# Kernel optimization log

Measured on AMD Instinct MI355X. Metric: run time of the kernel, lower is better.

Reference implementation:

```python
import jax, jax.numpy as jnp
import numpy as np
from jax import lax

B, T, H, M, K, Q, P = 32, 128, 256, 1000, 3, 4, 2  # batch, phones, hidden, max_mel_len, kernel, q_out, p_out


def _ln(x, g, b, eps=1e-5):
    mu = jnp.mean(x, -1, keepdims=True)
    var = jnp.mean((x - mu) ** 2, -1, keepdims=True)
    return (x - mu) * lax.rsqrt(var + eps) * g + b


def _forward(x, x_mask, x_dur, params):
    (proj_w, proj_b, conv_w, conv_b, conv_g, conv_beta,
     q_w1, q_b1, q_g, q_beta, q_w2, q_b2,
     p_w1, p_b1, p_g, p_beta, p_w2, p_b2,
     proj1_w, proj1_b, proj2_w, proj2_b, projo_w, projo_b) = params

    valid = (~x_mask).astype(x.dtype)[:, :, None]                      # (B,T,1), 1 = real phone
    # proj -> ConvBlock (shared between the w and c branches; dropout is identity in eval)
    h = x @ proj_w + proj_b                                            # (B,T,H)
    hc = lax.conv_general_dilated((h * valid).transpose(0, 2, 1), conv_w,
                                  (1,), 'SAME',
                                  dimension_numbers=('NCH', 'OIH', 'NCH'))
    hc = hc.transpose(0, 2, 1) + conv_b                                # (B,T,8)
    hc = jax.nn.silu(_ln(hc, conv_g, conv_beta)) * valid               # (B,T,8)

    mel_lens = jnp.minimum(jnp.round(jnp.sum(x_dur, -1)).astype(jnp.int32), M)
    mel_pad = jnp.arange(M)[None, :] >= mel_lens[:, None]              # (B,M) True = padded frame
    mask = x_mask[:, None, :] | mel_pad[:, :, None]                    # (B,M,T)

    e = jnp.cumsum(x_dur, -1)                                          # phone end times
    s = e - x_dur                                                      # phone start times
    t = jnp.arange(1, M + 1, dtype=x.dtype)
    E = jnp.where(mask, 0.0, e[:, None, :] - t[None, :, None])         # (B,M,T)
    S = jnp.where(mask, 0.0, t[None, :, None] - s[:, None, :])         # (B,M,T)

    feat = jnp.concatenate([jnp.broadcast_to(hc[:, None], (B, M, T, 8)),
                            S[..., None], E[..., None]], axis=-1)      # (B,M,T,10)

    # mlp_q scores -> masked softmax over phone axis
    sc = jax.nn.silu(_ln(feat @ q_w1 + q_b1, q_g, q_beta)) @ q_w2 + q_b2   # (B,M,T,Q)
    sc = jnp.where(x_mask[:, None, :, None], -jnp.inf, sc)
    w = jax.nn.softmax(sc, axis=2)
    w = jnp.where(mel_pad[:, :, None, None], 0.0, w)                   # (B,M,T,Q)

    # mlp_p per-(frame,phone) auxiliary features
    c = jax.nn.silu(_ln(feat @ p_w1 + p_b1, p_g, p_beta)) @ p_w2 + p_b2    # (B,M,T,P)

    # dual einsum combine (matches torch permute+view ordering: q-major then feature)
    wh = jnp.einsum('bmnq,bnh->bmqh', w, x).reshape(B, M, Q * H) @ proj1_w + proj1_b
    wc = jnp.einsum('bmnq,bmnp->bmqp', w, c).reshape(B, M, Q * P) @ proj2_w + proj2_b
    o = jnp.where(mel_pad[:, :, None], 0.0, wh + wc) @ projo_w + projo_b   # (B,M,2H)

    mel_mask = jnp.broadcast_to(mel_pad[:, :, None], (B, M, T))
    return o, mel_mask, mel_lens, jnp.transpose(w, (0, 3, 1, 2))


def setup_inputs() -> dict:
    key = jax.random.key(0)
    ks = jax.random.split(key, 16)
    x = jax.random.normal(ks[0], (B, T, H), jnp.float32)
    x_lengths = jax.random.randint(ks[1], (B,), T // 2, T + 1).at[0].set(T)
    x_mask = jnp.arange(T)[None, :] >= x_lengths[:, None]              # True = pad
    x_dur = jax.random.uniform(ks[2], (B, T), jnp.float32, 2.0, 10.0)
    x_dur = x_dur * (~x_mask)
    x_dur = x_dur.at[0].multiply(2.0)  # element 0 total duration > M -> static max_mel_len = M

    def xavier(k, shape):
        return jax.random.normal(k, shape, jnp.float32) * jnp.sqrt(2.0 / (shape[0] + shape[1]))

    return dict(
        x=x, x_mask=x_mask, x_dur=x_dur, x_lengths=x_lengths,
        proj_w=xavier(ks[3], (H, H)), proj_b=jnp.zeros((H,)),
        conv_w=jax.random.normal(ks[4], (8, H, K), jnp.float32) * 0.05, conv_b=jnp.zeros((8,)),
        conv_g=jnp.ones((8,)), conv_beta=jnp.zeros((8,)),
        q_w1=xavier(ks[5], (10, Q)), q_b1=jnp.zeros((Q,)),
        q_g=jnp.ones((Q,)), q_beta=jnp.zeros((Q,)),
        q_w2=xavier(ks[6], (Q, Q)), q_b2=jnp.zeros((Q,)),
        p_w1=xavier(ks[7], (10, P)), p_b1=jnp.zeros((P,)),
        p_g=jnp.ones((P,)), p_beta=jnp.zeros((P,)),
        p_w2=xavier(ks[8], (P, P)), p_b2=jnp.zeros((P,)),
        proj1_w=xavier(ks[9], (H * Q, H)), proj1_b=jnp.zeros((H,)),
        proj2_w=xavier(ks[10], (Q * P, H)), proj2_b=jnp.zeros((H,)),
        projo_w=xavier(ks[11], (H, 2 * H)), projo_b=jnp.zeros((2 * H,)),
    )


def reference(x, x_mask, x_dur, x_lengths,
              proj_w, proj_b, conv_w, conv_b, conv_g, conv_beta,
              q_w1, q_b1, q_g, q_beta, q_w2, q_b2,
              p_w1, p_b1, p_g, p_beta, p_w2, p_b2,
              proj1_w, proj1_b, proj2_w, proj2_b, projo_w, projo_b):
    params = (proj_w, proj_b, conv_w, conv_b, conv_g, conv_beta,
              q_w1, q_b1, q_g, q_beta, q_w2, q_b2,
              p_w1, p_b1, p_g, p_beta, p_w2, p_b2,
              proj1_w, proj1_b, proj2_w, proj2_b, projo_w, projo_b)
    return _forward(x, x_mask, x_dur, params)
```

## Files before the change

### kernel.cpp

```cpp
#include <hip/hip_runtime.h>
#include <math.h>

#define BB 32
#define TT 128
#define HH 256
#define MM 1000

typedef __attribute__((ext_vector_type(8))) short short8;
typedef __attribute__((ext_vector_type(4))) float floatx4;

__device__ inline void fma4(float4& a, const float4 b, float s) {
    a.x += b.x * s; a.y += b.y * s; a.z += b.z * s; a.w += b.w * s;
}

__device__ inline unsigned short f2bf(float f) {
    union { float f; unsigned int u; } c; c.f = f;
    unsigned int u = c.u;
    return (unsigned short)((u + 0x7FFFu + ((u >> 16) & 1u)) >> 16);
}

__device__ inline float bf2f(unsigned short h) {
    union { unsigned int u; float f; } c; c.u = ((unsigned int)h) << 16; return c.f;
}


__global__ void k_prep(const float* __restrict__ dur, float* __restrict__ e_cum,
                       int* __restrict__ ml_i, float* __restrict__ ml_out,
                       unsigned short* __restrict__ w_bf) {
    int b = blockIdx.x;
    int tid = threadIdx.x;
    #pragma unroll
    for (int q = 0; q < 4; ++q) {
        uint4* dst = (uint4*)(w_bf + (((size_t)(b * 4 + q)) * 1024 + 1000) * 128);
        for (int e = tid; e < 384; e += 64) dst[e] = make_uint4(0, 0, 0, 0);
    }
    if (tid == 0) {
        float run = 0.f;
        const float* d = dur + b * TT;
        float* e = e_cum + b * TT;
        for (int t = 0; t < TT; ++t) { run += d[t]; e[t] = run; }
        int ml = (int)rintf(run);
        if (ml > MM) ml = MM;
        if (ml < 0) ml = 0;
        ml_i[b] = ml;
        ml_out[b] = (float)ml;
    }
}

__global__ __launch_bounds__(256) void k_h(const float* __restrict__ x,
                                           const float* __restrict__ pw,
                                           const float* __restrict__ pb,
                                           float* __restrict__ h) {
    __shared__ float xs[16][HH];
    int blk = blockIdx.x;
    int b = blk >> 3, tt = blk & 7;
    int t0 = tt * 16;
    int tid = threadIdx.x;
    for (int e = tid; e < 16 * HH; e += 256) {
        int r = e >> 8, i = e & 255;
        xs[r][i] = x[(b * TT + t0 + r) * HH + i];
    }
    __syncthreads();
    int jg = tid & 63, rg = tid >> 6;
    int j4 = jg * 4;
    float4 bias = *(const float4*)(pb + j4);
    float4 acc[4];
    #pragma unroll
    for (int ri = 0; ri < 4; ++ri) acc[ri] = bias;
    #pragma unroll 4
    for (int i = 0; i < HH; ++i) {
        float4 wv = *(const float4*)(pw + i * HH + j4);
        #pragma unroll
        for (int ri = 0; ri < 4; ++ri) fma4(acc[ri], wv, xs[rg * 4 + ri][i]);
    }
    #pragma unroll
    for (int ri = 0; ri < 4; ++ri)
        *(float4*)(h + (b * TT + t0 + rg * 4 + ri) * HH + j4) = acc[ri];
}

__global__ __launch_bounds__(128) void k_conv(const float* __restrict__ h,
                                              const float* __restrict__ cw,
                                              const int* __restrict__ xlen,
                                              float* __restrict__ hcpre) {
    __shared__ float hs[18][257];
    __shared__ float cws[8][769];
    int blk = blockIdx.x;
    int b = blk >> 3, tt = blk & 7;
    int t0 = tt * 16;
    int tid = threadIdx.x;
    int L = xlen[b];
    for (int e = tid; e < 18 * 256; e += 128) {
        int r = e >> 8, i = e & 255;
        int t = t0 - 1 + r;
        float v = 0.f;
        if (t >= 0 && t < TT && t < L) v = h[((size_t)b * TT + t) * HH + i];
        hs[r][i] = v;
    }
    for (int e = tid; e < 6144; e += 128) {
        int o = e / 768, rem = e - o * 768;
        cws[o][rem] = cw[e];
    }
    __syncthreads();
    int o = tid >> 4, tl = tid & 15;
    float acc = 0.f;
    #pragma unroll
    for (int k = 0; k < 3; ++k) {
        const float* wr = &cws[o][k];
        const float* hr = hs[tl + k];
        #pragma unroll 8
        for (int i = 0; i < 256; ++i) acc += hr[i] * wr[i * 3];
    }
    hcpre[((size_t)b * TT + t0 + tl) * 8 + o] = acc;
}

__global__ __launch_bounds__(128) void k_bases(
    const float* __restrict__ hcpre, const float* __restrict__ cb,
    const float* __restrict__ cg, const float* __restrict__ cbeta,
    const float* __restrict__ qw1, const float* __restrict__ qb1,
    const float* __restrict__ pw1, const float* __restrict__ pb1,
    const float* __restrict__ e_cum, const float* __restrict__ dur,
    const int* __restrict__ xlen,
    float* __restrict__ baseq, float* __restrict__ basep) {
    int b = blockIdx.x;
    int t = threadIdx.x;
    int L = xlen[b];
    float v[8];
    float mu = 0.f;
    #pragma unroll
    for (int o = 0; o < 8; ++o) { v[o] = hcpre[(b * TT + t) * 8 + o] + cb[o]; mu += v[o]; }
    mu *= 0.125f;
    float var = 0.f;
    #pragma unroll
    for (int o = 0; o < 8; ++o) { float d = v[o] - mu; var += d * d; }
    var *= 0.125f;
    float rs = 1.0f / sqrtf(var + 1e-5f);
    float valid = (t < L) ? 1.f : 0.f;
    #pragma unroll
    for (int o = 0; o < 8; ++o) {
        float a = (v[o] - mu) * rs * cg[o] + cbeta[o];
        v[o] = a / (1.f + expf(-a)) * valid;
    }
    float e = e_cum[b * TT + t];
    float s_ = e - dur[b * TT + t];
    #pragma unroll
    for (int j = 0; j < 4; ++j) {
        float acc = qb1[j];
        #pragma unroll
        for (int o = 0; o < 8; ++o) acc += v[o] * qw1[o * 4 + j];
        acc += e * qw1[9 * 4 + j] - s_ * qw1[8 * 4 + j];
        baseq[(b * TT + t) * 4 + j] = acc;
    }
    #pragma unroll
    for (int j = 0; j < 2; ++j) {
        float acc = pb1[j];
        #pragma unroll
        for (int o = 0; o < 8; ++o) acc += v[o] * pw1[o * 2 + j];
        acc += e * pw1[9 * 2 + j] - s_ * pw1[8 * 2 + j];
        basep[(b * TT + t) * 2 + j] = acc;
    }
}

__global__ __launch_bounds__(256) void k_wsoft(
    const float* __restrict__ baseq, const float* __restrict__ basep,
    const float* __restrict__ qw1, const float* __restrict__ qg,
    const float* __restrict__ qbeta, const float* __restrict__ qw2,
    const float* __restrict__ qb2,
    const float* __restrict__ pw1, const float* __restrict__ pg,
    const float* __restrict__ pbeta, const float* __restrict__ pw2,
    const float* __restrict__ pb2,
    const int* __restrict__ xlen, const int* __restrict__ ml_i,
    float* __restrict__ w_out, float* __restrict__ mm_out,
    float* __restrict__ wc8, unsigned short* __restrict__ w_bf) {
    int blk = blockIdx.x;
    int b = blk / 250;
    int mg = blk - b * 250;
    int wv = threadIdx.x >> 6, lane = threadIdx.x & 63;
    int m = mg * 4 + wv;
    int ml = ml_i[b];
    int t1 = lane, t2 = lane + 64;
    bool pad = (m >= ml);
    size_t mmbase = ((size_t)b * MM + m) * TT;
    mm_out[mmbase + t1] = pad ? 1.f : 0.f;
    mm_out[mmbase + t2] = pad ? 1.f : 0.f;
    if (pad) {
        #pragma unroll
        for (int q = 0; q < 4; ++q) {
            size_t wb = ((size_t)(b * 4 + q) * MM + m) * TT;
            w_out[wb + t1] = 0.f;
            w_out[wb + t2] = 0.f;
            unsigned short* wbq = w_bf + (((size_t)(b * 4 + q)) * 1024 + m) * 128;
            wbq[t1] = 0; wbq[t2] = 0;
        }
        if (lane == 0) {
            #pragma unroll
            for (int r = 0; r < 8; ++r) wc8[((size_t)b * MM + m) * 8 + r] = 0.f;
        }
        return;
    }
    int L = xlen[b];
    float mp1 = (float)(m + 1);
    float dq[4];
    #pragma unroll
    for (int j = 0; j < 4; ++j) dq[j] = mp1 * (qw1[8 * 4 + j] - qw1[9 * 4 + j]);

    float sc1[4], sc2[4];
    float c1v[2], c2v[2];
    #pragma unroll
    for (int half = 0; half < 2; ++half) {
        int t = half ? t2 : t1;
        float* sc = half ? sc2 : sc1;
        float* cv = half ? c2v : c1v;
        if (t < L) {
            float4 bq = *(const float4*)(baseq + ((size_t)b * TT + t) * 4);
            float z[4] = {bq.x + dq[0], bq.y + dq[1], bq.z + dq[2], bq.w + dq[3]};
            float mu = 0.25f * (z[0] + z[1] + z[2] + z[3]);
            float var = 0.f;
            #pragma unroll
            for (int j = 0; j < 4; ++j) { float d = z[j] - mu; var += d * d; }
            var *= 0.25f;
            float rs = 1.f / sqrtf(var + 1e-5f);
            float a[4];
            #pragma unroll
            for (int j = 0; j < 4; ++j) {
                float av = (z[j] - mu) * rs * qg[j] + qbeta[j];
                a[j] = av / (1.f + expf(-av));
            }
            #pragma unroll
            for (int q = 0; q < 4; ++q) {
                float s = qb2[q];
                #pragma unroll
                for (int j = 0; j < 4; ++j) s += a[j] * qw2[j * 4 + q];
                sc[q] = s;
            }
            float z0 = basep[((size_t)b * TT + t) * 2 + 0] + mp1 * (pw1[16] - pw1[18]);
            float z1 = basep[((size_t)b * TT + t) * 2 + 1] + mp1 * (pw1[17] - pw1[19]);
            float pmu = 0.5f * (z0 + z1);
            float d0 = z0 - pmu, d1 = z1 - pmu;
            float pvar = 0.5f * (d0 * d0 + d1 * d1);
            float prs = 1.f / sqrtf(pvar + 1e-5f);
            float a0 = d0 * prs * pg[0] + pbeta[0];
            float a1 = d1 * prs * pg[1] + pbeta[1];
            a0 = a0 / (1.f + expf(-a0));
            a1 = a1 / (1.f + expf(-a1));
            cv[0] = pb2[0] + a0 * pw2[0] + a1 * pw2[2];
            cv[1] = pb2[1] + a0 * pw2[1] + a1 * pw2[3];
        } else {
            sc[0] = sc[1] = sc[2] = sc[3] = -__builtin_inff();
            cv[0] = cv[1] = 0.f;
        }
    }
    float w1[4], w2[4];
    #pragma unroll
    for (int q = 0; q < 4; ++q) {
        float mx = fmaxf(sc1[q], sc2[q]);
        #pragma unroll
        for (int off = 32; off > 0; off >>= 1) mx = fmaxf(mx, __shfl_xor(mx, off, 64));
        float e1 = expf(sc1[q] - mx);
        float e2 = expf(sc2[q] - mx);
        float s = e1 + e2;
        #pragma unroll
        for (int off = 32; off > 0; off >>= 1) s += __shfl_xor(s, off, 64);
        w1[q] = e1 / s;
        w2[q] = e2 / s;
        size_t wb = ((size_t)(b * 4 + q) * MM + m) * TT;
        w_out[wb + t1] = w1[q];
        w_out[wb + t2] = w2[q];
        unsigned short* wbq = w_bf + (((size_t)(b * 4 + q)) * 1024 + m) * 128;
        wbq[t1] = f2bf(w1[q]);
        wbq[t2] = f2bf(w2[q]);
    }
    float red[8];
    #pragma unroll
    for (int r8 = 0; r8 < 8; ++r8) {
        int q = r8 >> 1, p = r8 & 1;
        float v = w1[q] * c1v[p] + w2[q] * c2v[p];
        #pragma unroll
        for (int off = 32; off > 0; off >>= 1) v += __shfl_xor(v, off, 64);
        red[r8] = v;
    }
    if (lane == 0) {
        #pragma unroll
        for (int r8 = 0; r8 < 8; ++r8) wc8[((size_t)b * MM + m) * 8 + r8] = red[r8];
    }
}

__global__ __launch_bounds__(256) void k_pw_part(const float* __restrict__ p1w,
                                                 const float* __restrict__ po,
                                                 float* __restrict__ PWpart) {
    __shared__ float S[16][64];
    int blk = blockIdx.x;
    int ks = blk & 3, colT = (blk >> 2) & 7, ht = blk >> 5;
    int q = colT >> 1, j0 = (colT & 1) * 256;
    int h0 = ht * 16, k0 = ks * 64;
    int tid = threadIdx.x;
    for (int e = tid; e < 1024; e += 256) {
        int r = e >> 6, c = e & 63;
        S[r][c] = p1w[(q * 256 + h0 + r) * 256 + k0 + c];
    }
    __syncthreads();
    int jg = tid & 63, rg = tid >> 6;
    int jcol = j0 + jg * 4;
    float4 acc[4];
    #pragma unroll
    for (int r = 0; r < 4; ++r) acc[r] = make_float4(0, 0, 0, 0);
    float4 nb = *(const float4*)(po + (size_t)k0 * 512 + jcol);
    for (int c = 0; c < 64; ++c) {
        float4 cur = nb;
        if (c < 63) nb = *(const float4*)(po + (size_t)(k0 + c + 1) * 512 + jcol);
        #pragma unroll
        for (int r = 0; r < 4; ++r) fma4(acc[r], cur, S[rg * 4 + r][c]);
    }
    #pragma unroll
    for (int r = 0; r < 4; ++r) {
        int hh = h0 + rg * 4 + r;
        *(float4*)(PWpart + (size_t)ks * 524288 + hh * 2048 + q * 512 + jcol) = acc[r];
    }
}

__global__ __launch_bounds__(256) void k_pwt(const float* __restrict__ PWpart,
                                             unsigned short* __restrict__ pwh,
                                             unsigned short* __restrict__ pwl) {
    __shared__ float S[64][65];
    int blk = blockIdx.x;
    int nt = blk & 31, ct = blk >> 5;
    int c0 = ct * 64, n0 = nt * 64;
    int tid = threadIdx.x;
    for (int e = tid; e < 4096; e += 256) {
        int cc = e >> 6, nn = e & 63;
        size_t off = (size_t)(c0 + cc) * 2048 + n0 + nn;
        float v = PWpart[off] + PWpart[524288 + off]
                + PWpart[2 * 524288 + off] + PWpart[3 * 524288 + off];
        S[cc][nn] = v;
    }
    __syncthreads();
    for (int e = tid; e < 4096; e += 256) {
        int nn = e >> 6, cc = e & 63;
        float v = S[cc][nn];
        unsigned short h = f2bf(v);
        size_t d = (size_t)(n0 + nn) * 256 + c0 + cc;
        pwh[d] = h;
        pwl[d] = f2bf(v - bf2f(h));
    }
}

__global__ __launch_bounds__(256) void k_xcvt(const float* __restrict__ x,
                                              unsigned short* __restrict__ xh,
                                              unsigned short* __restrict__ xl) {
    int idx = (blockIdx.x * 256 + threadIdx.x) * 4;
    float4 v = *(const float4*)(x + idx);
    float vv[4] = {v.x, v.y, v.z, v.w};
    union { unsigned short us[4]; uint2 u; } hi, lo;
    #pragma unroll
    for (int k = 0; k < 4; ++k) {
        unsigned short h = f2bf(vv[k]);
        hi.us[k] = h;
        lo.us[k] = f2bf(vv[k] - bf2f(h));
    }
    *(uint2*)(xh + idx) = hi.u;
    *(uint2*)(xl + idx) = lo.u;
}

__global__ __launch_bounds__(512) void k_small(const float* __restrict__ p2w,
    const float* __restrict__ po, const float* __restrict__ p1b,
    const float* __restrict__ p2b, const float* __restrict__ pob,
    float* __restrict__ P2o, float* __restrict__ bvec) {
    int j = threadIdx.x;
    float acc[9];
    #pragma unroll
    for (int r = 0; r < 9; ++r) acc[r] = 0.f;
    for (int c = 0; c < HH; ++c) {
        float pv = po[c * 512 + j];
        #pragma unroll
        for (int r = 0; r < 8; ++r) acc[r] += p2w[r * HH + c] * pv;
        acc[8] += (p1b[c] + p2b[c]) * pv;
    }
    #pragma unroll
    for (int r = 0; r < 8; ++r) P2o[r * 512 + j] = acc[r];
    bvec[j] = acc[8] + pob[j];
}

__device__ inline int swzk(int row, int chunk) {
    return row * 32 + ((chunk ^ ((row >> 1) & 3)) << 3);
}

__global__ __launch_bounds__(256) void k_A2m(const unsigned short* __restrict__ xh,
                                             const unsigned short* __restrict__ xl,
                                             const unsigned short* __restrict__ pwh,
                                             const unsigned short* __restrict__ pwl,
                                             unsigned short* __restrict__ A2T) {
    __shared__ __align__(16) unsigned short SM[16384];
    unsigned short* Ah = SM;
    unsigned short* Al = SM + 4096;
    unsigned short* Bh = SM + 8192;
    unsigned short* Bl = SM + 12288;
    int blk = blockIdx.x;
    int b = blk >> 4, nt = blk & 15;
    int n0 = nt * 128;
    int tid = threadIdx.x;
    int lane = tid & 63, wv = tid >> 6;
    int wm = wv & 1, wn = wv >> 1;

    floatx4 acc[16];
    #pragma unroll
    for (int i = 0; i < 16; ++i) acc[i] = (floatx4){0.f, 0.f, 0.f, 0.f};

    int srow = tid >> 1, shalf = tid & 1;
    const unsigned short* gxh = xh + ((size_t)(b * TT + srow) * 256 + shalf * 16);
    const unsigned short* gxl = xl + ((size_t)(b * TT + srow) * 256 + shalf * 16);
    const unsigned short* gph = pwh + ((size_t)(n0 + srow) * 256 + shalf * 16);
    const unsigned short* gpl = pwl + ((size_t)(n0 + srow) * 256 + shalf * 16);
    int wAd0 = swzk(srow, 2 * shalf);
    int wAd1 = swzk(srow, 2 * shalf + 1);

    int ra = wm * 64 + (lane & 15);
    int rb = wn * 64 + (lane & 15);
    int cq = lane >> 4;

    for (int kc = 0; kc < 256; kc += 32) {
        uint4 a0 = *(const uint4*)(gxh + kc);
        uint4 a1 = *(const uint4*)(gxh + kc + 8);
        uint4 a2 = *(const uint4*)(gxl + kc);
        uint4 a3 = *(const uint4*)(gxl + kc + 8);
        uint4 b0 = *(const uint4*)(gph + kc);
        uint4 b1 = *(const uint4*)(gph + kc + 8);
        uint4 b2 = *(const uint4*)(gpl + kc);
        uint4 b3 = *(const uint4*)(gpl + kc + 8);
        *(uint4*)&Ah[wAd0] = a0; *(uint4*)&Ah[wAd1] = a1;
        *(uint4*)&Al[wAd0] = a2; *(uint4*)&Al[wAd1] = a3;
        *(uint4*)&Bh[wAd0] = b0; *(uint4*)&Bh[wAd1] = b1;
        *(uint4*)&Bl[wAd0] = b2; *(uint4*)&Bl[wAd1] = b3;
        __syncthreads();
        short8 afh[4], afl[4], bfh[4], bfl[4];
        #pragma unroll
        for (int i = 0; i < 4; ++i) {
            afh[i] = *(const short8*)&Ah[swzk(ra + i * 16, cq)];
            afl[i] = *(const short8*)&Al[swzk(ra + i * 16, cq)];
            bfh[i] = *(const short8*)&Bh[swzk(rb + i * 16, cq)];
            bfl[i] = *(const short8*)&Bl[swzk(rb + i * 16, cq)];
        }
        #pragma unroll
        for (int i = 0; i < 4; ++i)
            #pragma unroll
            for (int j = 0; j < 4; ++j) {
                floatx4 c = acc[i * 4 + j];
                c = __builtin_amdgcn_mfma_f32_16x16x32_bf16(afh[i], bfh[j], c, 0, 0, 0);
                c = __builtin_amdgcn_mfma_f32_16x16x32_bf16(afh[i], bfl[j], c, 0, 0, 0);
                c = __builtin_amdgcn_mfma_f32_16x16x32_bf16(afl[i], bfh[j], c, 0, 0, 0);
                acc[i * 4 + j] = c;
            }
        __syncthreads();
    }

    unsigned short* OT = SM;
    #pragma unroll
    for (int i = 0; i < 4; ++i)
        #pragma unroll
        for (int j = 0; j < 4; ++j) {
            int nloc = wn * 64 + j * 16 + (lane & 15);
            int tb = wm * 64 + i * 16 + ((lane >> 4) << 2);
            union { unsigned short us[4]; uint2 v; } pk;
            #pragma unroll
            for (int r = 0; r < 4; ++r) pk.us[r] = f2bf(acc[i * 4 + j][r]);
            int chunk = tb >> 3, sub = tb & 7;
            *(uint2*)&OT[nloc * 128 + (((chunk ^ (nloc & 15)) << 3) | sub)] = pk.v;
        }
    __syncthreads();
    int q = n0 >> 9, jb = n0 & 511;
    for (int u = tid; u < 2048; u += 256) {
        int nrow = u >> 4, seg = u & 15;
        uint4 v = *(const uint4*)&OT[nrow * 128 + ((seg ^ (nrow & 15)) << 3)];
        *(uint4*)(A2T + (((size_t)(b * 4 + q) * 512) + jb + nrow) * 128 + seg * 8) = v;
    }
}

__global__ __launch_bounds__(256, 2) void k_main(
    const unsigned short* __restrict__ w_bf, const unsigned short* __restrict__ A2T,
    const float* __restrict__ wc8, const float* __restrict__ P2o,
    const float* __restrict__ bvec, const float* __restrict__ pob,
    const int* __restrict__ ml_i, float* __restrict__ o_out) {
    __shared__ __align__(16) unsigned short Asm[2][128 * 40];
    __shared__ __align__(16) unsigned short Bsm[2][128 * 40];
    int wgid = blockIdx.x;
    int blk = (wgid & 7) * 128 + (wgid >> 3);
    int nt = blk & 3, mt = (blk >> 2) & 7, b = blk >> 5;
    int m0 = mt * 128, n0 = nt * 128;
    int tid = threadIdx.x;
    int ml = ml_i[b];

    if (m0 >= ml) {
        float* pb_s = (float*)&Asm[0][0];
        if (tid < 128) pb_s[tid] = pob[n0 + tid];
        __syncthreads();
        int col4 = (tid & 31) * 4;
        float4 pv = *(const float4*)&pb_s[col4];
        for (int r = tid >> 5; r < 128; r += 8) {
            int m = m0 + r;
            if (m < MM)
                *(float4*)(o_out + ((size_t)b * MM + m) * 512 + n0 + col4) = pv;
        }
        return;
    }

    int lane = tid & 63, wv = tid >> 6;
    int wm = wv & 1, wn = wv >> 1;

    floatx4 acc[16];
    #pragma unroll
    for (int i = 0; i < 16; ++i) acc[i] = (floatx4){0.f, 0.f, 0.f, 0.f};

    int rl = lane >> 4;
    int cl = lane & 15;
    int ra = wm * 64 + cl;
    int rb = wn * 64 + cl;

    int srow = tid >> 2, schunk = tid & 3;
    int doff = srow * 40 + schunk * 8;
    const size_t bq4 = (size_t)b * 4;

    #pragma unroll
    for (int j = 0; j < 2; ++j) {
        int row = srow + j * 64;
        uint4 va = *(const uint4*)(w_bf + ((bq4 + 0) * 1024 + m0 + row) * 128 + schunk * 8);
        uint4 vb = *(const uint4*)(A2T + ((bq4 + 0) * 512 + n0 + row) * 128 + schunk * 8);
        *(uint4*)&Asm[0][doff + j * 2560] = va;
        *(uint4*)&Bsm[0][doff + j * 2560] = vb;
    }
    __syncthreads();

    int cur = 0;
    for (int s = 0; s < 16; ++s) {
        uint4 la[2], lb[2];
        if (s < 15) {
            int q = (s + 1) >> 2, koff = ((s + 1) & 3) * 32;
            #pragma unroll
            for (int j = 0; j < 2; ++j) {
                int row = srow + j * 64;
                la[j] = *(const uint4*)(w_bf +
                    ((bq4 + q) * 1024 + m0 + row) * 128 + koff + schunk * 8);
                lb[j] = *(const uint4*)(A2T +
                    ((bq4 + q) * 512 + n0 + row) * 128 + koff + schunk * 8);
            }
        }
        {
            int co = rl * 8;
            short8 af[4], bfr[4];
            #pragma unroll
            for (int i = 0; i < 4; ++i)
                af[i] = *(const short8*)&Asm[cur][(ra + i * 16) * 40 + co];
            #pragma unroll
            for (int j2 = 0; j2 < 4; ++j2)
                bfr[j2] = *(const short8*)&Bsm[cur][(rb + j2 * 16) * 40 + co];
            #pragma unroll
            for (int i = 0; i < 4; ++i)
                #pragma unroll
                for (int j2 = 0; j2 < 4; ++j2)
                    acc[i * 4 + j2] = __builtin_amdgcn_mfma_f32_16x16x32_bf16(
                        af[i], bfr[j2], acc[i * 4 + j2], 0, 0, 0);
        }
        if (s < 15) {
            #pragma unroll
            for (int j = 0; j < 2; ++j) {
                *(uint4*)&Asm[cur ^ 1][doff + j * 2560] = la[j];
                *(uint4*)&Bsm[cur ^ 1][doff + j * 2560] = lb[j];
            }
        }
        __syncthreads();
        cur ^= 1;
    }

    float* wc8s = (float*)&Asm[0][0];
    float* P2os = (float*)&Bsm[0][0];
    float* bvs  = (float*)&Bsm[0][0] + 1024;
    float* pobs = (float*)&Bsm[0][0] + 1152;
    for (int e = tid; e < 1024; e += 256) {
        int mm_ = e >> 3, r = e & 7;
        int m = m0 + mm_;
        wc8s[e] = (m < MM) ? wc8[((size_t)b * MM + m) * 8 + r] : 0.f;
    }
    for (int e = tid; e < 1024; e += 256) {
        int r = e >> 7, j = e & 127;
        P2os[e] = P2o[r * 512 + n0 + j];
    }
    if (tid < 128) {
        bvs[tid] = bvec[n0 + tid];
        pobs[tid] = pob[n0 + tid];
    }
    __syncthreads();
    #pragma unroll
    for (int i = 0; i < 4; ++i) {
        #pragma unroll
        for (int j = 0; j < 4; ++j) {
            int nloc = wn * 64 + j * 16 + (lane & 15);
            #pragma unroll
            for (int reg = 0; reg < 4; ++reg) {
                int mloc = wm * 64 + i * 16 + (lane >> 4) * 4 + reg;
                int m = m0 + mloc;
                if (m >= MM) continue;
                float v;
                if (m < ml) {
                    v = acc[i * 4 + j][reg] + bvs[nloc];
                    #pragma unroll
                    for (int r8 = 0; r8 < 8; ++r8)
                        v += wc8s[mloc * 8 + r8] * P2os[r8 * 128 + nloc];
                } else {
                    v = pobs[nloc];
                }
                o_out[((size_t)b * MM + m) * 512 + n0 + nloc] = v;
            }
        }
    }
}

extern "C" void kernel_launch(void* const* d_in, const int* in_sizes, int n_in,
                              void* d_out, int out_size, void* d_ws, size_t ws_size,
                              hipStream_t stream) {
    (void)in_sizes; (void)n_in; (void)out_size; (void)ws_size;
    const float* x      = (const float*)d_in[0];
    const float* dur    = (const float*)d_in[2];
    const int*   xlen   = (const int*)d_in[3];
    const float* proj_w = (const float*)d_in[4];
    const float* proj_b = (const float*)d_in[5];
    const float* conv_w = (const float*)d_in[6];
    const float* conv_b = (const float*)d_in[7];
    const float* conv_g = (const float*)d_in[8];
    const float* conv_be= (const float*)d_in[9];
    const float* q_w1   = (const float*)d_in[10];
    const float* q_b1   = (const float*)d_in[11];
    const float* q_g    = (const float*)d_in[12];
    const float* q_be   = (const float*)d_in[13];
    const float* q_w2   = (const float*)d_in[14];
    const float* q_b2   = (const float*)d_in[15];
    const float* p_w1   = (const float*)d_in[16];
    const float* p_b1   = (const float*)d_in[17];
    const float* p_g    = (const float*)d_in[18];
    const float* p_be   = (const float*)d_in[19];
    const float* p_w2   = (const float*)d_in[20];
    const float* p_b2   = (const float*)d_in[21];
    const float* p1w    = (const float*)d_in[22];
    const float* p1b    = (const float*)d_in[23];
    const float* p2w    = (const float*)d_in[24];
    const float* p2b    = (const float*)d_in[25];
    const float* pow_   = (const float*)d_in[26];
    const float* pob    = (const float*)d_in[27];

    float* ws    = (float*)d_ws;
    float* e_cum = ws + 0;
    float* hcpre = ws + 4096;
    float* baseq = ws + 36864;
    float* basep = ws + 53248;
    float* h     = ws + 61440;
    unsigned short* x_hi = (unsigned short*)(ws + 61440);
    unsigned short* x_lo = (unsigned short*)(ws + 585728);
    unsigned short* pw_h = (unsigned short*)(ws + 1110016);
    unsigned short* pw_l = (unsigned short*)(ws + 1372160);
    unsigned short* A2T = (unsigned short*)(ws + 1634304);
    float* wc8   = ws + 5828608;
    float* P2o   = ws + 6084608;
    float* bvec  = ws + 6088704;
    int*   ml_i  = (int*)(ws + 6089216);
    float* PWpart= ws + 6090752;
    unsigned short* w_bf = (unsigned short*)(ws + 8187904);

    float* o_out  = (float*)d_out;
    float* mm_out = o_out + 16384000;
    float* ml_out = o_out + 20480000;
    float* w_out  = o_out + 20480032;

    k_prep<<<dim3(BB), dim3(64), 0, stream>>>(dur, e_cum, ml_i, ml_out, w_bf);
    k_h<<<dim3(BB * 8), dim3(256), 0, stream>>>(x, proj_w, proj_b, h);
    k_conv<<<dim3(BB * 8), dim3(128), 0, stream>>>(h, conv_w, xlen, hcpre);
    k_xcvt<<<dim3(1024), dim3(256), 0, stream>>>(x, x_hi, x_lo);
    k_bases<<<dim3(BB), dim3(128), 0, stream>>>(hcpre, conv_b, conv_g, conv_be,
                                                q_w1, q_b1, p_w1, p_b1,
                                                e_cum, dur, xlen, baseq, basep);
    k_pw_part<<<dim3(512), dim3(256), 0, stream>>>(p1w, pow_, PWpart);
    k_pwt<<<dim3(128), dim3(256), 0, stream>>>(PWpart, pw_h, pw_l);
    k_small<<<dim3(1), dim3(512), 0, stream>>>(p2w, pow_, p1b, p2b, pob, P2o, bvec);
    k_A2m<<<dim3(512), dim3(256), 0, stream>>>(x_hi, x_lo, pw_h, pw_l, A2T);
    k_wsoft<<<dim3(BB * 250), dim3(256), 0, stream>>>(baseq, basep,
                                                      q_w1, q_g, q_be, q_w2, q_b2,
                                                      p_w1, p_g, p_be, p_w2, p_b2,
                                                      xlen, ml_i, w_out, mm_out, wc8, w_bf);
    k_main<<<dim3(BB * 32), dim3(256), 0, stream>>>(w_bf, A2T, wc8, P2o, bvec,
                                                    pob, ml_i, o_out);
}
```

Before: 397.7 us.

## Merge nine small preprocessing kernels into three block-dispatched launches by dependency level

Independent preprocessing kernels are grouped by dependency level into three kernels (kF1, kF2, kF3) that branch on block index to run the original per-kernel work. This cuts launch count and idle gaps between tiny kernels, and lets independent work such as the proj matmul, the PW partial products, the x conversion and the prep share the GPU at once. The x_hi/x_lo buffers move to a new workspace offset because they previously aliased h, which is now written in the same launch. Shared memory per block becomes the union of the merged kernels, and some branches leave threads idle (e.g., the conv part uses 128 of 256 threads).

```diff
diff --git a/kernel.cpp b/kernel.cpp
--- a/kernel.cpp
+++ b/kernel.cpp
@@ -24,96 +24,197 @@
 }
 
 
-__global__ void k_prep(const float* __restrict__ dur, float* __restrict__ e_cum,
-                       int* __restrict__ ml_i, float* __restrict__ ml_out,
-                       unsigned short* __restrict__ w_bf) {
-    int b = blockIdx.x;
+__global__ __launch_bounds__(256) void kF1(
+    const float* __restrict__ x, const float* __restrict__ pw_h_,
+    const float* __restrict__ pb_h, float* __restrict__ h,
+    const float* __restrict__ p1w, const float* __restrict__ po,
+    float* __restrict__ PWpart,
+    unsigned short* __restrict__ xh, unsigned short* __restrict__ xl,
+    const float* __restrict__ dur, float* __restrict__ e_cum,
+    int* __restrict__ ml_i, float* __restrict__ ml_out,
+    unsigned short* __restrict__ w_bf) {
+    __shared__ __align__(16) float S1[4096];
+    int gb = blockIdx.x;
     int tid = threadIdx.x;
-    #pragma unroll
-    for (int q = 0; q < 4; ++q) {
-        uint4* dst = (uint4*)(w_bf + (((size_t)(b * 4 + q)) * 1024 + 1000) * 128);
-        for (int e = tid; e < 384; e += 64) dst[e] = make_uint4(0, 0, 0, 0);
-    }
-    if (tid == 0) {
-        float run = 0.f;
-        const float* d = dur + b * TT;
-        float* e = e_cum + b * TT;
-        for (int t = 0; t < TT; ++t) { run += d[t]; e[t] = run; }
-        int ml = (int)rintf(run);
-        if (ml > MM) ml = MM;
-        if (ml < 0) ml = 0;
-        ml_i[b] = ml;
-        ml_out[b] = (float)ml;
-    }
-}
-
-__global__ __launch_bounds__(256) void k_h(const float* __restrict__ x,
-                                           const float* __restrict__ pw,
-                                           const float* __restrict__ pb,
-                                           float* __restrict__ h) {
-    __shared__ float xs[16][HH];
-    int blk = blockIdx.x;
-    int b = blk >> 3, tt = blk & 7;
-    int t0 = tt * 16;
+
+    if (gb < 256) {
+        float (*xs)[HH] = (float(*)[HH])S1;
+        int b = gb >> 3, tt = gb & 7;
+        int t0 = tt * 16;
+        for (int e = tid; e < 16 * HH; e += 256) {
+            int r = e >> 8, i = e & 255;
+            xs[r][i] = x[(b * TT + t0 + r) * HH + i];
+        }
+        __syncthreads();
+        int jg = tid & 63, rg = tid >> 6;
+        int j4 = jg * 4;
+        float4 bias = *(const float4*)(pb_h + j4);
+        float4 acc[4];
+        #pragma unroll
+        for (int ri = 0; ri < 4; ++ri) acc[ri] = bias;
+        #pragma unroll 4
+        for (int i = 0; i < HH; ++i) {
+            float4 wv = *(const float4*)(pw_h_ + i * HH + j4);
+            #pragma unroll
+            for (int ri = 0; ri < 4; ++ri) fma4(acc[ri], wv, xs[rg * 4 + ri][i]);
+        }
+        #pragma unroll
+        for (int ri = 0; ri < 4; ++ri)
+            *(float4*)(h + (b * TT + t0 + rg * 4 + ri) * HH + j4) = acc[ri];
+    } else if (gb < 768) {
+        float (*S)[64] = (float(*)[64])S1;
+        int blk = gb - 256;
+        int ks = blk & 3, colT = (blk >> 2) & 7, ht = blk >> 5;
+        int q = colT >> 1, j0 = (colT & 1) * 256;
+        int h0 = ht * 16, k0 = ks * 64;
+        for (int e = tid; e < 1024; e += 256) {
+            int r = e >> 6, c = e & 63;
+            S[r][c] = p1w[(q * 256 + h0 + r) * 256 + k0 + c];
+        }
+        __syncthreads();
+        int jg = tid & 63, rg = tid >> 6;
+        int jcol = j0 + jg * 4;
+        float4 acc[4];
+        #pragma unroll
+        for (int r = 0; r < 4; ++r) acc[r] = make_float4(0, 0, 0, 0);
+        float4 nb = *(const float4*)(po + (size_t)k0 * 512 + jcol);
+        for (int c = 0; c < 64; ++c) {
+            float4 cur = nb;
+            if (c < 63) nb = *(const float4*)(po + (size_t)(k0 + c + 1) * 512 + jcol);
+            #pragma unroll
+            for (int r = 0; r < 4; ++r) fma4(acc[r], cur, S[rg * 4 + r][c]);
+        }
+        #pragma unroll
+        for (int r = 0; r < 4; ++r) {
+            int hh = h0 + rg * 4 + r;
+            *(float4*)(PWpart + (size_t)ks * 524288 + hh * 2048 + q * 512 + jcol) = acc[r];
+        }
+    } else if (gb < 1792) {
+        int idx = ((gb - 768) * 256 + tid) * 4;
+        float4 v = *(const float4*)(x + idx);
+        float vv[4] = {v.x, v.y, v.z, v.w};
+        union { unsigned short us[4]; uint2 u; } hi, lo;
+        #pragma unroll
+        for (int k = 0; k < 4; ++k) {
+            unsigned short hv = f2bf(vv[k]);
+            hi.us[k] = hv;
+            lo.us[k] = f2bf(vv[k] - bf2f(hv));
+        }
+        *(uint2*)(xh + idx) = hi.u;
+        *(uint2*)(xl + idx) = lo.u;
+    } else {
+        int b = gb - 1792;
+        if (tid < 64) {
+            #pragma unroll
+            for (int q = 0; q < 4; ++q) {
+                uint4* dst = (uint4*)(w_bf + (((size_t)(b * 4 + q)) * 1024 + 1000) * 128);
+                for (int e = tid; e < 384; e += 64) dst[e] = make_uint4(0, 0, 0, 0);
+            }
+            if (tid == 0) {
+                float run = 0.f;
+                const float* d = dur + b * TT;
+                float* e = e_cum + b * TT;
+                for (int t = 0; t < TT; ++t) { run += d[t]; e[t] = run; }
+                int ml = (int)rintf(run);
+                if (ml > MM) ml = MM;
+                if (ml < 0) ml = 0;
+                ml_i[b] = ml;
+                ml_out[b] = (float)ml;
+            }
+        }
+    }
+}
+
+__global__ __launch_bounds__(256) void kF2(
+    const float* __restrict__ h, const float* __restrict__ cw,
+    const int* __restrict__ xlen, float* __restrict__ hcpre,
+    const float* __restrict__ PWpart,
+    unsigned short* __restrict__ pwh, unsigned short* __restrict__ pwl,
+    const float* __restrict__ p2w, const float* __restrict__ po,
+    const float* __restrict__ p1b, const float* __restrict__ p2b,
+    const float* __restrict__ pob,
+    float* __restrict__ P2o, float* __restrict__ bvec) {
+    __shared__ __align__(16) float S2[10778];
+    int gb = blockIdx.x;
     int tid = threadIdx.x;
-    for (int e = tid; e < 16 * HH; e += 256) {
-        int r = e >> 8, i = e & 255;
-        xs[r][i] = x[(b * TT + t0 + r) * HH + i];
-    }
-    __syncthreads();
-    int jg = tid & 63, rg = tid >> 6;
-    int j4 = jg * 4;
-    float4 bias = *(const float4*)(pb + j4);
-    float4 acc[4];
-    #pragma unroll
-    for (int ri = 0; ri < 4; ++ri) acc[ri] = bias;
-    #pragma unroll 4
-    for (int i = 0; i < HH; ++i) {
-        float4 wv = *(const float4*)(pw + i * HH + j4);
-        #pragma unroll
-        for (int ri = 0; ri < 4; ++ri) fma4(acc[ri], wv, xs[rg * 4 + ri][i]);
-    }
-    #pragma unroll
-    for (int ri = 0; ri < 4; ++ri)
-        *(float4*)(h + (b * TT + t0 + rg * 4 + ri) * HH + j4) = acc[ri];
-}
-
-__global__ __launch_bounds__(128) void k_conv(const float* __restrict__ h,
-                                              const float* __restrict__ cw,
-                                              const int* __restrict__ xlen,
-                                              float* __restrict__ hcpre) {
-    __shared__ float hs[18][257];
-    __shared__ float cws[8][769];
-    int blk = blockIdx.x;
-    int b = blk >> 3, tt = blk & 7;
-    int t0 = tt * 16;
-    int tid = threadIdx.x;
-    int L = xlen[b];
-    for (int e = tid; e < 18 * 256; e += 128) {
-        int r = e >> 8, i = e & 255;
-        int t = t0 - 1 + r;
-        float v = 0.f;
-        if (t >= 0 && t < TT && t < L) v = h[((size_t)b * TT + t) * HH + i];
-        hs[r][i] = v;
-    }
-    for (int e = tid; e < 6144; e += 128) {
-        int o = e / 768, rem = e - o * 768;
-        cws[o][rem] = cw[e];
-    }
-    __syncthreads();
-    int o = tid >> 4, tl = tid & 15;
-    float acc = 0.f;
-    #pragma unroll
-    for (int k = 0; k < 3; ++k) {
-        const float* wr = &cws[o][k];
-        const float* hr = hs[tl + k];
-        #pragma unroll 8
-        for (int i = 0; i < 256; ++i) acc += hr[i] * wr[i * 3];
-    }
-    hcpre[((size_t)b * TT + t0 + tl) * 8 + o] = acc;
-}
-
-__global__ __launch_bounds__(128) void k_bases(
+
+    if (gb < 256) {
+        float (*hs)[257] = (float(*)[257])S2;
+        float (*cws)[769] = (float(*)[769])(S2 + 4626);
+        int b = gb >> 3, tt = gb & 7;
+        int t0 = tt * 16;
+        int L = xlen[b];
+        for (int e = tid; e < 18 * 256; e += 256) {
+            int r = e >> 8, i = e & 255;
+            int t = t0 - 1 + r;
+            float v = 0.f;
+            if (t >= 0 && t < TT && t < L) v = h[((size_t)b * TT + t) * HH + i];
+            hs[r][i] = v;
+        }
+        for (int e = tid; e < 6144; e += 256) {
+            int o = e / 768, rem = e - o * 768;
+            cws[o][rem] = cw[e];
+        }
+        __syncthreads();
+        if (tid < 128) {
+            int o = tid >> 4, tl = tid & 15;
+            float acc = 0.f;
+            #pragma unroll
+            for (int k = 0; k < 3; ++k) {
+                const float* wr = &cws[o][k];
+                const float* hr = hs[tl + k];
+                #pragma unroll 8
+                for (int i = 0; i < 256; ++i) acc += hr[i] * wr[i * 3];
+            }
+            hcpre[((size_t)b * TT + t0 + tl) * 8 + o] = acc;
+        }
+    } else if (gb < 384) {
+        float (*S)[65] = (float(*)[65])S2;
+        int blk = gb - 256;
+        int nt = blk & 31, ct = blk >> 5;
+        int c0 = ct * 64, n0 = nt * 64;
+        for (int e = tid; e < 4096; e += 256) {
+            int cc = e >> 6, nn = e & 63;
+            size_t off = (size_t)(c0 + cc) * 2048 + n0 + nn;
+            float v = PWpart[off] + PWpart[524288 + off]
+                    + PWpart[2 * 524288 + off] + PWpart[3 * 524288 + off];
+            S[cc][nn] = v;
+        }
+        __syncthreads();
+        for (int e = tid; e < 4096; e += 256) {
+            int nn = e >> 6, cc = e & 63;
+            float v = S[cc][nn];
+            unsigned short hv = f2bf(v);
+            size_t d = (size_t)(n0 + nn) * 256 + c0 + cc;
+            pwh[d] = hv;
+            pwl[d] = f2bf(v - bf2f(hv));
+        }
+    } else {
+        for (int j = tid; j < 512; j += 256) {
+            float acc[9];
+            #pragma unroll
+            for (int r = 0; r < 9; ++r) acc[r] = 0.f;
+            for (int c = 0; c < HH; ++c) {
+                float pv = po[c * 512 + j];
+                #pragma unroll
+                for (int r = 0; r < 8; ++r) acc[r] += p2w[r * HH + c] * pv;
+                acc[8] += (p1b[c] + p2b[c]) * pv;
+            }
+            #pragma unroll
+            for (int r = 0; r < 8; ++r) P2o[r * 512 + j] = acc[r];
+            bvec[j] = acc[8] + pob[j];
+        }
+    }
+}
+
+__device__ inline int swzk(int row, int chunk) {
+    return row * 32 + ((chunk ^ ((row >> 1) & 3)) << 3);
+}
+
+__global__ __launch_bounds__(256) void kF3(
+    const unsigned short* __restrict__ xh, const unsigned short* __restrict__ xl,
+    const unsigned short* __restrict__ pwh, const unsigned short* __restrict__ pwl,
+    unsigned short* __restrict__ A2T,
     const float* __restrict__ hcpre, const float* __restrict__ cb,
     const float* __restrict__ cg, const float* __restrict__ cbeta,
     const float* __restrict__ qw1, const float* __restrict__ qb1,
@@ -121,42 +222,133 @@
     const float* __restrict__ e_cum, const float* __restrict__ dur,
     const int* __restrict__ xlen,
     float* __restrict__ baseq, float* __restrict__ basep) {
-    int b = blockIdx.x;
-    int t = threadIdx.x;
-    int L = xlen[b];
-    float v[8];
-    float mu = 0.f;
-    #pragma unroll
-    for (int o = 0; o < 8; ++o) { v[o] = hcpre[(b * TT + t) * 8 + o] + cb[o]; mu += v[o]; }
-    mu *= 0.125f;
-    float var = 0.f;
-    #pragma unroll
-    for (int o = 0; o < 8; ++o) { float d = v[o] - mu; var += d * d; }
-    var *= 0.125f;
-    float rs = 1.0f / sqrtf(var + 1e-5f);
-    float valid = (t < L) ? 1.f : 0.f;
-    #pragma unroll
-    for (int o = 0; o < 8; ++o) {
-        float a = (v[o] - mu) * rs * cg[o] + cbeta[o];
-        v[o] = a / (1.f + expf(-a)) * valid;
-    }
-    float e = e_cum[b * TT + t];
-    float s_ = e - dur[b * TT + t];
-    #pragma unroll
-    for (int j = 0; j < 4; ++j) {
-        float acc = qb1[j];
-        #pragma unroll
-        for (int o = 0; o < 8; ++o) acc += v[o] * qw1[o * 4 + j];
-        acc += e * qw1[9 * 4 + j] - s_ * qw1[8 * 4 + j];
-        baseq[(b * TT + t) * 4 + j] = acc;
-    }
-    #pragma unroll
-    for (int j = 0; j < 2; ++j) {
-        float acc = pb1[j];
-        #pragma unroll
-        for (int o = 0; o < 8; ++o) acc += v[o] * pw1[o * 2 + j];
-        acc += e * pw1[9 * 2 + j] - s_ * pw1[8 * 2 + j];
-        basep[(b * TT + t) * 2 + j] = acc;
+    __shared__ __align__(16) unsigned short SM[16384];
+    int gblk = blockIdx.x;
+    int tid = threadIdx.x;
+
+    if (gblk >= 512) {
+        int b = gblk - 512;
+        int t = tid;
+        if (t < 128) {
+            int L = xlen[b];
+            float v[8];
+            float mu = 0.f;
+            #pragma unroll
+            for (int o = 0; o < 8; ++o) { v[o] = hcpre[(b * TT + t) * 8 + o] + cb[o]; mu += v[o]; }
+            mu *= 0.125f;
+            float var = 0.f;
+            #pragma unroll
+            for (int o = 0; o < 8; ++o) { float d = v[o] - mu; var += d * d; }
+            var *= 0.125f;
+            float rs = 1.0f / sqrtf(var + 1e-5f);
+            float valid = (t < L) ? 1.f : 0.f;
+            #pragma unroll
+            for (int o = 0; o < 8; ++o) {
+                float a = (v[o] - mu) * rs * cg[o] + cbeta[o];
+                v[o] = a / (1.f + expf(-a)) * valid;
+            }
+            float e = e_cum[b * TT + t];
+            float s_ = e - dur[b * TT + t];
+            #pragma unroll
+            for (int j = 0; j < 4; ++j) {
+                float acc = qb1[j];
+                #pragma unroll
+                for (int o = 0; o < 8; ++o) acc += v[o] * qw1[o * 4 + j];
+                acc += e * qw1[9 * 4 + j] - s_ * qw1[8 * 4 + j];
+                baseq[(b * TT + t) * 4 + j] = acc;
+            }
+            #pragma unroll
+            for (int j = 0; j < 2; ++j) {
+                float acc = pb1[j];
+                #pragma unroll
+                for (int o = 0; o < 8; ++o) acc += v[o] * pw1[o * 2 + j];
+                acc += e * pw1[9 * 2 + j] - s_ * pw1[8 * 2 + j];
+                basep[(b * TT + t) * 2 + j] = acc;
+            }
+        }
+        return;
+    }
+
+    unsigned short* Ah = SM;
+    unsigned short* Al = SM + 4096;
+    unsigned short* Bh = SM + 8192;
+    unsigned short* Bl = SM + 12288;
+    int blk = gblk;
+    int b = blk >> 4, nt = blk & 15;
+    int n0 = nt * 128;
+    int lane = tid & 63, wv = tid >> 6;
+    int wm = wv & 1, wn = wv >> 1;
+
+    floatx4 acc[16];
+    #pragma unroll
+    for (int i = 0; i < 16; ++i) acc[i] = (floatx4){0.f, 0.f, 0.f, 0.f};
+
+    int srow = tid >> 1, shalf = tid & 1;
+    const unsigned short* gxh = xh + ((size_t)(b * TT + srow) * 256 + shalf * 16);
+    const unsigned short* gxl = xl + ((size_t)(b * TT + srow) * 256 + shalf * 16);
+    const unsigned short* gph = pwh + ((size_t)(n0 + srow) * 256 + shalf * 16);
+    const unsigned short* gpl = pwl + ((size_t)(n0 + srow) * 256 + shalf * 16);
+    int wAd0 = swzk(srow, 2 * shalf);
+    int wAd1 = swzk(srow, 2 * shalf + 1);
+
+    int ra = wm * 64 + (lane & 15);
+    int rb = wn * 64 + (lane & 15);
+    int cq = lane >> 4;
+
+    for (int kc = 0; kc < 256; kc += 32) {
+        uint4 a0 = *(const uint4*)(gxh + kc);
+        uint4 a1 = *(const uint4*)(gxh + kc + 8);
+        uint4 a2 = *(const uint4*)(gxl + kc);
+        uint4 a3 = *(const uint4*)(gxl + kc + 8);
+        uint4 b0 = *(const uint4*)(gph + kc);
+        uint4 b1 = *(const uint4*)(gph + kc + 8);
+        uint4 b2 = *(const uint4*)(gpl + kc);
+        uint4 b3 = *(const uint4*)(gpl + kc + 8);
+        *(uint4*)&Ah[wAd0] = a0; *(uint4*)&Ah[wAd1] = a1;
+        *(uint4*)&Al[wAd0] = a2; *(uint4*)&Al[wAd1] = a3;
+        *(uint4*)&Bh[wAd0] = b0; *(uint4*)&Bh[wAd1] = b1;
+        *(uint4*)&Bl[wAd0] = b2; *(uint4*)&Bl[wAd1] = b3;
+        __syncthreads();
+        short8 afh[4], afl[4], bfh[4], bfl[4];
+        #pragma unroll
+        for (int i = 0; i < 4; ++i) {
+            afh[i] = *(const short8*)&Ah[swzk(ra + i * 16, cq)];
+            afl[i] = *(const short8*)&Al[swzk(ra + i * 16, cq)];
+            bfh[i] = *(const short8*)&Bh[swzk(rb + i * 16, cq)];
+            bfl[i] = *(const short8*)&Bl[swzk(rb + i * 16, cq)];
+        }
+        #pragma unroll
+        for (int i = 0; i < 4; ++i)
+            #pragma unroll
+            for (int j = 0; j < 4; ++j) {
+                floatx4 c = acc[i * 4 + j];
+                c = __builtin_amdgcn_mfma_f32_16x16x32_bf16(afh[i], bfh[j], c, 0, 0, 0);
+                c = __builtin_amdgcn_mfma_f32_16x16x32_bf16(afh[i], bfl[j], c, 0, 0, 0);
+                c = __builtin_amdgcn_mfma_f32_16x16x32_bf16(afl[i], bfh[j], c, 0, 0, 0);
+                acc[i * 4 + j] = c;
+            }
+        __syncthreads();
+    }
+
+    unsigned short* OT = SM;
+    #pragma unroll
+    for (int i = 0; i < 4; ++i)
+        #pragma unroll
+        for (int j = 0; j < 4; ++j) {
+            int nloc = wn * 64 + j * 16 + (lane & 15);
+            int tb = wm * 64 + i * 16 + ((lane >> 4) << 2);
+            union { unsigned short us[4]; uint2 v; } pk;
+            #pragma unroll
+            for (int r = 0; r < 4; ++r) pk.us[r] = f2bf(acc[i * 4 + j][r]);
+            int chunk = tb >> 3, sub = tb & 7;
+            *(uint2*)&OT[nloc * 128 + (((chunk ^ (nloc & 15)) << 3) | sub)] = pk.v;
+        }
+    __syncthreads();
+    int q = n0 >> 9, jb = n0 & 511;
+    for (int u = tid; u < 2048; u += 256) {
+        int nrow = u >> 4, seg = u & 15;
+        uint4 v = *(const uint4*)&OT[nrow * 128 + ((seg ^ (nrow & 15)) << 3)];
+        *(uint4*)(A2T + (((size_t)(b * 4 + q) * 512) + jb + nrow) * 128 + seg * 8) = v;
     }
 }
 
@@ -281,195 +473,6 @@
     if (lane == 0) {
         #pragma unroll
         for (int r8 = 0; r8 < 8; ++r8) wc8[((size_t)b * MM + m) * 8 + r8] = red[r8];
-    }
-}
-
-__global__ __launch_bounds__(256) void k_pw_part(const float* __restrict__ p1w,
-                                                 const float* __restrict__ po,
-                                                 float* __restrict__ PWpart) {
-    __shared__ float S[16][64];
-    int blk = blockIdx.x;
-    int ks = blk & 3, colT = (blk >> 2) & 7, ht = blk >> 5;
-    int q = colT >> 1, j0 = (colT & 1) * 256;
-    int h0 = ht * 16, k0 = ks * 64;
-    int tid = threadIdx.x;
-    for (int e = tid; e < 1024; e += 256) {
-        int r = e >> 6, c = e & 63;
-        S[r][c] = p1w[(q * 256 + h0 + r) * 256 + k0 + c];
-    }
-    __syncthreads();
-    int jg = tid & 63, rg = tid >> 6;
-    int jcol = j0 + jg * 4;
-    float4 acc[4];
-    #pragma unroll
-    for (int r = 0; r < 4; ++r) acc[r] = make_float4(0, 0, 0, 0);
-    float4 nb = *(const float4*)(po + (size_t)k0 * 512 + jcol);
-    for (int c = 0; c < 64; ++c) {
-        float4 cur = nb;
-        if (c < 63) nb = *(const float4*)(po + (size_t)(k0 + c + 1) * 512 + jcol);
-        #pragma unroll
-        for (int r = 0; r < 4; ++r) fma4(acc[r], cur, S[rg * 4 + r][c]);
-    }
-    #pragma unroll
-    for (int r = 0; r < 4; ++r) {
-        int hh = h0 + rg * 4 + r;
-        *(float4*)(PWpart + (size_t)ks * 524288 + hh * 2048 + q * 512 + jcol) = acc[r];
-    }
-}
-
-__global__ __launch_bounds__(256) void k_pwt(const float* __restrict__ PWpart,
-                                             unsigned short* __restrict__ pwh,
-                                             unsigned short* __restrict__ pwl) {
-    __shared__ float S[64][65];
-    int blk = blockIdx.x;
-    int nt = blk & 31, ct = blk >> 5;
-    int c0 = ct * 64, n0 = nt * 64;
-    int tid = threadIdx.x;
-    for (int e = tid; e < 4096; e += 256) {
-        int cc = e >> 6, nn = e & 63;
-        size_t off = (size_t)(c0 + cc) * 2048 + n0 + nn;
-        float v = PWpart[off] + PWpart[524288 + off]
-                + PWpart[2 * 524288 + off] + PWpart[3 * 524288 + off];
-        S[cc][nn] = v;
-    }
-    __syncthreads();
-    for (int e = tid; e < 4096; e += 256) {
-        int nn = e >> 6, cc = e & 63;
-        float v = S[cc][nn];
-        unsigned short h = f2bf(v);
-        size_t d = (size_t)(n0 + nn) * 256 + c0 + cc;
-        pwh[d] = h;
-        pwl[d] = f2bf(v - bf2f(h));
-    }
-}
-
-__global__ __launch_bounds__(256) void k_xcvt(const float* __restrict__ x,
-                                              unsigned short* __restrict__ xh,
-                                              unsigned short* __restrict__ xl) {
-    int idx = (blockIdx.x * 256 + threadIdx.x) * 4;
-    float4 v = *(const float4*)(x + idx);
-    float vv[4] = {v.x, v.y, v.z, v.w};
-    union { unsigned short us[4]; uint2 u; } hi, lo;
-    #pragma unroll
-    for (int k = 0; k < 4; ++k) {
-        unsigned short h = f2bf(vv[k]);
-        hi.us[k] = h;
-        lo.us[k] = f2bf(vv[k] - bf2f(h));
-    }
-    *(uint2*)(xh + idx) = hi.u;
-    *(uint2*)(xl + idx) = lo.u;
-}
-
-__global__ __launch_bounds__(512) void k_small(const float* __restrict__ p2w,
-    const float* __restrict__ po, const float* __restrict__ p1b,
-    const float* __restrict__ p2b, const float* __restrict__ pob,
-    float* __restrict__ P2o, float* __restrict__ bvec) {
-    int j = threadIdx.x;
-    float acc[9];
-    #pragma unroll
-    for (int r = 0; r < 9; ++r) acc[r] = 0.f;
-    for (int c = 0; c < HH; ++c) {
-        float pv = po[c * 512 + j];
-        #pragma unroll
-        for (int r = 0; r < 8; ++r) acc[r] += p2w[r * HH + c] * pv;
-        acc[8] += (p1b[c] + p2b[c]) * pv;
-    }
-    #pragma unroll
-    for (int r = 0; r < 8; ++r) P2o[r * 512 + j] = acc[r];
-    bvec[j] = acc[8] + pob[j];
-}
-
-__device__ inline int swzk(int row, int chunk) {
-    return row * 32 + ((chunk ^ ((row >> 1) & 3)) << 3);
-}
-
-__global__ __launch_bounds__(256) void k_A2m(const unsigned short* __restrict__ xh,
-                                             const unsigned short* __restrict__ xl,
-                                             const unsigned short* __restrict__ pwh,
-                                             const unsigned short* __restrict__ pwl,
-                                             unsigned short* __restrict__ A2T) {
-    __shared__ __align__(16) unsigned short SM[16384];
-    unsigned short* Ah = SM;
-    unsigned short* Al = SM + 4096;
-    unsigned short* Bh = SM + 8192;
-    unsigned short* Bl = SM + 12288;
-    int blk = blockIdx.x;
-    int b = blk >> 4, nt = blk & 15;
-    int n0 = nt * 128;
-    int tid = threadIdx.x;
-    int lane = tid & 63, wv = tid >> 6;
-    int wm = wv & 1, wn = wv >> 1;
-
-    floatx4 acc[16];
-    #pragma unroll
-    for (int i = 0; i < 16; ++i) acc[i] = (floatx4){0.f, 0.f, 0.f, 0.f};
-
-    int srow = tid >> 1, shalf = tid & 1;
-    const unsigned short* gxh = xh + ((size_t)(b * TT + srow) * 256 + shalf * 16);
-    const unsigned short* gxl = xl + ((size_t)(b * TT + srow) * 256 + shalf * 16);
-    const unsigned short* gph = pwh + ((size_t)(n0 + srow) * 256 + shalf * 16);
-    const unsigned short* gpl = pwl + ((size_t)(n0 + srow) * 256 + shalf * 16);
-    int wAd0 = swzk(srow, 2 * shalf);
-    int wAd1 = swzk(srow, 2 * shalf + 1);
-
-    int ra = wm * 64 + (lane & 15);
-    int rb = wn * 64 + (lane & 15);
-    int cq = lane >> 4;
-
-    for (int kc = 0; kc < 256; kc += 32) {
-        uint4 a0 = *(const uint4*)(gxh + kc);
-        uint4 a1 = *(const uint4*)(gxh + kc + 8);
-        uint4 a2 = *(const uint4*)(gxl + kc);
-        uint4 a3 = *(const uint4*)(gxl + kc + 8);
-        uint4 b0 = *(const uint4*)(gph + kc);
-        uint4 b1 = *(const uint4*)(gph + kc + 8);
-        uint4 b2 = *(const uint4*)(gpl + kc);
-        uint4 b3 = *(const uint4*)(gpl + kc + 8);
-        *(uint4*)&Ah[wAd0] = a0; *(uint4*)&Ah[wAd1] = a1;
-        *(uint4*)&Al[wAd0] = a2; *(uint4*)&Al[wAd1] = a3;
-        *(uint4*)&Bh[wAd0] = b0; *(uint4*)&Bh[wAd1] = b1;
-        *(uint4*)&Bl[wAd0] = b2; *(uint4*)&Bl[wAd1] = b3;
-        __syncthreads();
-        short8 afh[4], afl[4], bfh[4], bfl[4];
-        #pragma unroll
-        for (int i = 0; i < 4; ++i) {
-            afh[i] = *(const short8*)&Ah[swzk(ra + i * 16, cq)];
-            afl[i] = *(const short8*)&Al[swzk(ra + i * 16, cq)];
-            bfh[i] = *(const short8*)&Bh[swzk(rb + i * 16, cq)];
-            bfl[i] = *(const short8*)&Bl[swzk(rb + i * 16, cq)];
-        }
-        #pragma unroll
-        for (int i = 0; i < 4; ++i)
-            #pragma unroll
-            for (int j = 0; j < 4; ++j) {
-                floatx4 c = acc[i * 4 + j];
-                c = __builtin_amdgcn_mfma_f32_16x16x32_bf16(afh[i], bfh[j], c, 0, 0, 0);
-                c = __builtin_amdgcn_mfma_f32_16x16x32_bf16(afh[i], bfl[j], c, 0, 0, 0);
-                c = __builtin_amdgcn_mfma_f32_16x16x32_bf16(afl[i], bfh[j], c, 0, 0, 0);
-                acc[i * 4 + j] = c;
-            }
-        __syncthreads();
-    }
-
-    unsigned short* OT = SM;
-    #pragma unroll
-    for (int i = 0; i < 4; ++i)
-        #pragma unroll
-        for (int j = 0; j < 4; ++j) {
-            int nloc = wn * 64 + j * 16 + (lane & 15);
-            int tb = wm * 64 + i * 16 + ((lane >> 4) << 2);
-            union { unsigned short us[4]; uint2 v; } pk;
-            #pragma unroll
-            for (int r = 0; r < 4; ++r) pk.us[r] = f2bf(acc[i * 4 + j][r]);
-            int chunk = tb >> 3, sub = tb & 7;
-            *(uint2*)&OT[nloc * 128 + (((chunk ^ (nloc & 15)) << 3) | sub)] = pk.v;
-        }
-    __syncthreads();
-    int q = n0 >> 9, jb = n0 & 511;
-    for (int u = tid; u < 2048; u += 256) {
-        int nrow = u >> 4, seg = u & 15;
-        uint4 v = *(const uint4*)&OT[nrow * 128 + ((seg ^ (nrow & 15)) << 3)];
-        *(uint4*)(A2T + (((size_t)(b * 4 + q) * 512) + jb + nrow) * 128 + seg * 8) = v;
     }
 }
 
@@ -649,8 +652,6 @@
     float* baseq = ws + 36864;
     float* basep = ws + 53248;
     float* h     = ws + 61440;
-    unsigned short* x_hi = (unsigned short*)(ws + 61440);
-    unsigned short* x_lo = (unsigned short*)(ws + 585728);
     unsigned short* pw_h = (unsigned short*)(ws + 1110016);
     unsigned short* pw_l = (unsigned short*)(ws + 1372160);
     unsigned short* A2T = (unsigned short*)(ws + 1634304);
@@ -660,23 +661,25 @@
     int*   ml_i  = (int*)(ws + 6089216);
     float* PWpart= ws + 6090752;
     unsigned short* w_bf = (unsigned short*)(ws + 8187904);
+    unsigned short* x_hi = (unsigned short*)(ws + 16576512);
+    unsigned short* x_lo = (unsigned short*)(ws + 17100800);
 
     float* o_out  = (float*)d_out;
     float* mm_out = o_out + 16384000;
     float* ml_out = o_out + 20480000;
     float* w_out  = o_out + 20480032;
 
-    k_prep<<<dim3(BB), dim3(64), 0, stream>>>(dur, e_cum, ml_i, ml_out, w_bf);
-    k_h<<<dim3(BB * 8), dim3(256), 0, stream>>>(x, proj_w, proj_b, h);
-    k_conv<<<dim3(BB * 8), dim3(128), 0, stream>>>(h, conv_w, xlen, hcpre);
-    k_xcvt<<<dim3(1024), dim3(256), 0, stream>>>(x, x_hi, x_lo);
-    k_bases<<<dim3(BB), dim3(128), 0, stream>>>(hcpre, conv_b, conv_g, conv_be,
-                                                q_w1, q_b1, p_w1, p_b1,
-                                                e_cum, dur, xlen, baseq, basep);
-    k_pw_part<<<dim3(512), dim3(256), 0, stream>>>(p1w, pow_, PWpart);
-    k_pwt<<<dim3(128), dim3(256), 0, stream>>>(PWpart, pw_h, pw_l);
-    k_small<<<dim3(1), dim3(512), 0, stream>>>(p2w, pow_, p1b, p2b, pob, P2o, bvec);
-    k_A2m<<<dim3(512), dim3(256), 0, stream>>>(x_hi, x_lo, pw_h, pw_l, A2T);
+    kF1<<<dim3(1824), dim3(256), 0, stream>>>(x, proj_w, proj_b, h,
+                                              p1w, pow_, PWpart,
+                                              x_hi, x_lo,
+                                              dur, e_cum, ml_i, ml_out, w_bf);
+    kF2<<<dim3(385), dim3(256), 0, stream>>>(h, conv_w, xlen, hcpre,
+                                             PWpart, pw_h, pw_l,
+                                             p2w, pow_, p1b, p2b, pob, P2o, bvec);
+    kF3<<<dim3(544), dim3(256), 0, stream>>>(x_hi, x_lo, pw_h, pw_l, A2T,
+                                             hcpre, conv_b, conv_g, conv_be,
+                                             q_w1, q_b1, p_w1, p_b1,
+                                             e_cum, dur, xlen, baseq, basep);
     k_wsoft<<<dim3(BB * 250), dim3(256), 0, stream>>>(baseq, basep,
                                                       q_w1, q_g, q_be, q_w2, q_b2,
                                                       p_w1, p_g, p_be, p_w2, p_b2,
```

Measured after the change: 373.4 us. -6.1%, faster.
